# Kernel optimization log

Measured on AMD Instinct MI355X. Metric: run time of the kernel, lower is better.

The kernel has to match this reference:

```python
import jax, jax.numpy as jnp
import numpy as np
from jax import lax

B0, C0, H0, W0 = 4, 128, 48, 48
GR = 32  # growth rate
NL = 4   # dense layers


def conv1x1(x, w, b):
    # w: [O, Cin], x: [B, Cin, H, W]
    return jnp.einsum('oc,bchw->bohw', w, x) + b[None, :, None, None]


def conv3x3(x, w, b):
    y = lax.conv_general_dilated(x, w, (1, 1), [(1, 1), (1, 1)],
                                 dimension_numbers=('NCHW', 'OIHW', 'NCHW'))
    return y + b[None, :, None, None]


def batchnorm(x, g, b, eps=1e-5):
    # training-mode BatchNorm2d: batch statistics over (B, H, W)
    mu = jnp.mean(x, axis=(0, 2, 3), keepdims=True)
    var = jnp.var(x, axis=(0, 2, 3), keepdims=True)
    return (x - mu) * lax.rsqrt(var + eps) * g[None, :, None, None] + b[None, :, None, None]


def apply_rope(x):
    B, C, H, W = x.shape
    half = C // 2
    theta = 1.0 / (10000.0 ** (jnp.arange(half, dtype=x.dtype) / half))
    # pos_emb[h, w, j] = (h + w) * theta[j]
    pos = (jnp.arange(H, dtype=x.dtype)[:, None, None]
           + jnp.arange(W, dtype=x.dtype)[None, :, None]) * theta
    cos = jnp.cos(pos).transpose(2, 0, 1)  # [half, H, W]
    sin = jnp.sin(pos).transpose(2, 0, 1)
    xr = x.reshape(B, half, 2, H, W)
    x_re, x_im = xr[:, :, 0], xr[:, :, 1]
    rr = x_re * cos - x_im * sin
    ri = x_re * sin + x_im * cos
    return jnp.stack([rr, ri], axis=2).reshape(B, C, H, W)


def setup_inputs() -> dict:
    key = jax.random.key(0)
    ks = iter(jax.random.split(key, 64))
    def nrm(shape, s=0.05):
        return jax.random.normal(next(ks), shape, jnp.float32) * s
    C = C0
    dc = C + NL * GR  # 256 dense-block output channels
    hid = 4 * C
    d = {
        'x': jax.random.normal(next(ks), (B0, C0, H0, W0), jnp.float32),
        'r_w': nrm((C, C)), 'r_b': jnp.zeros((C,), jnp.float32),
        'k_w': nrm((C, C)), 'k_b': jnp.zeros((C,), jnp.float32),
        'v_w': nrm((C, C)), 'v_b': jnp.zeros((C,), jnp.float32),
        'wc1_w': nrm((C // 4, C, 3, 3)), 'wc1_b': jnp.zeros((C // 4,), jnp.float32),
        'wc2_w': nrm((C, C // 4)), 'wc2_b': jnp.zeros((C,), jnp.float32),
        'u': nrm((C,), 0.1),
        'sn1_w': nrm((dc // 4, dc)), 'sn1_b': jnp.zeros((dc // 4,), jnp.float32),
        'sn2_w': nrm((dc, dc // 4)), 'sn2_b': jnp.zeros((dc,), jnp.float32),
        'lb_w': nrm((C // 4, dc)), 'lb_b': jnp.zeros((C // 4,), jnp.float32),
        'ld_w': nrm((C // 4, dc)), 'ld_b': jnp.zeros((C // 4,), jnp.float32),
        'ps_w': nrm((C, C // 4)), 'ps_b': jnp.zeros((C,), jnp.float32),
        'pq_w': nrm((C, C)), 'pq_b': jnp.zeros((C,), jnp.float32),
        'fc1_w': nrm((hid, C)), 'fc1_b': jnp.zeros((hid,), jnp.float32),
        'fc2_w': nrm((C, hid)), 'fc2_b': jnp.zeros((C,), jnp.float32),
    }
    for i in range(NL):
        cin = C + i * GR
        d[f'db_g{i}'] = jnp.ones((cin,), jnp.float32)
        d[f'db_b{i}'] = jnp.zeros((cin,), jnp.float32)
        d[f'db_w{i}'] = nrm((GR, cin, 3, 3))
        d[f'db_cb{i}'] = jnp.zeros((GR,), jnp.float32)
    return d


def _forward(x, r_w, r_b, k_w, k_b, v_w, v_b, wc1_w, wc1_b, wc2_w, wc2_b, u,
             db_g0, db_b0, db_w0, db_cb0, db_g1, db_b1, db_w1, db_cb1,
             db_g2, db_b2, db_w2, db_cb2, db_g3, db_b3, db_w3, db_cb3,
             sn1_w, sn1_b, sn2_w, sn2_b, lb_w, lb_b, ld_w, ld_b,
             ps_w, ps_b, pq_w, pq_b, fc1_w, fc1_b, fc2_w, fc2_b):
    B, C, H, W = x.shape
    N = H * W
    # decay gate w (hidden is None so it multiplies zeros, kept for fidelity)
    w_gate = jax.nn.sigmoid(conv1x1(jax.nn.relu(conv3x3(x, wc1_w, wc1_b)), wc2_w, wc2_b)).reshape(B, C, N)
    x_rope = apply_rope(x)
    r = jax.nn.sigmoid(conv1x1(x, r_w, r_b))
    k = conv1x1(x_rope, k_w, k_b).reshape(B, C, N)
    v = conv1x1(x_rope, v_w, v_b).reshape(B, C, N)
    zeros = jnp.zeros_like(k)
    new_num = zeros * jnp.exp(-w_gate) + k * v
    new_den = zeros * jnp.exp(-w_gate) + k
    eu = jnp.exp(u)[None, :, None]
    wkv = ((new_num + eu * k * v) / (new_den + eu * k)).reshape(B, C, H, W)
    recursive_output = r * wkv
    # dense block (concat-growth)
    feats = x
    for g, bb, wt, cb in ((db_g0, db_b0, db_w0, db_cb0), (db_g1, db_b1, db_w1, db_cb1),
                          (db_g2, db_b2, db_w2, db_cb2), (db_g3, db_b3, db_w3, db_cb3)):
        h = jax.nn.relu(batchnorm(feats, g, bb))
        feats = jnp.concatenate([feats, conv3x3(h, wt, cb)], axis=1)
    df = feats  # [B, C+4*GR, H, W]
    # adaptive spiking neuron
    tau = jnp.mean(jax.nn.sigmoid(conv1x1(jax.nn.relu(conv1x1(df, sn1_w, sn1_b)), sn2_w, sn2_b)),
                   axis=(2, 3), keepdims=True)
    spike_prob = jax.nn.sigmoid((df - 1.0) * 5.0)
    sf = spike_prob * (df * jnp.exp(-1.0 / (tau + 1e-6))) + (1.0 - spike_prob) * df
    # first attention over N tokens, channels = C//4
    Bf = conv1x1(sf, lb_w, lb_b).reshape(B, -1, N)
    Df = conv1x1(sf, ld_w, ld_b).reshape(B, -1, N)
    attn = jax.nn.softmax(jnp.einsum('bcn,bcm->bnm', Bf, Bf), axis=-1)
    att1 = jnp.einsum('bnm,bcm->bcn', attn, Df).reshape(B, -1, H, W)
    spike_output = conv1x1(att1, ps_w, ps_b)
    combined = recursive_output + spike_output
    # second attention (k/v convs are shared with WKV path)
    Q = conv1x1(combined, pq_w, pq_b).reshape(B, C, N)
    K = conv1x1(combined, k_w, k_b).reshape(B, C, N)
    V = conv1x1(combined, v_w, v_b).reshape(B, C, N)
    scores = jnp.einsum('bcn,bcm->bnm', Q, K) / jnp.sqrt(jnp.asarray(C, x.dtype))
    aw = jax.nn.softmax(scores, axis=-1)
    att2 = jnp.einsum('bnm,bcm->bcn', aw, V).reshape(B, C, H, W)
    x1 = x + att2
    out = x1 + conv1x1(jax.nn.relu(conv1x1(x1, fc1_w, fc1_b)) ** 2, fc2_w, fc2_b)
    return out, new_num, new_den


def reference(x, r_w, r_b, k_w, k_b, v_w, v_b, wc1_w, wc1_b, wc2_w, wc2_b, u,
              db_g0, db_b0, db_w0, db_cb0, db_g1, db_b1, db_w1, db_cb1,
              db_g2, db_b2, db_w2, db_cb2, db_g3, db_b3, db_w3, db_cb3,
              sn1_w, sn1_b, sn2_w, sn2_b, lb_w, lb_b, ld_w, ld_b,
              ps_w, ps_b, pq_w, pq_b, fc1_w, fc1_b, fc2_w, fc2_b):
    return _forward(x, r_w, r_b, k_w, k_b, v_w, v_b, wc1_w, wc1_b, wc2_w, wc2_b, u,
                    db_g0, db_b0, db_w0, db_cb0, db_g1, db_b1, db_w1, db_cb1,
                    db_g2, db_b2, db_w2, db_cb2, db_g3, db_b3, db_w3, db_cb3,
                    sn1_w, sn1_b, sn2_w, sn2_b, lb_w, lb_b, ld_w, ld_b,
                    ps_w, ps_b, pq_w, pq_b, fc1_w, fc1_b, fc2_w, fc2_b)
```

## Files before the change

### kernel.cpp

```cpp
#include <hip/hip_runtime.h>
#include <math.h>

#define BB 4
#define CC 128
#define HH 48
#define WW 48
#define NSP (HH*WW)
#define DCC 256
#define BCN (BB*CC*NSP)
#define KS 4

typedef float f32x4 __attribute__((ext_vector_type(4)));
typedef __bf16 bf16x8 __attribute__((ext_vector_type(8)));
typedef __bf16 bf16x4 __attribute__((ext_vector_type(4)));

__device__ __forceinline__ float sigmf(float v) { return 1.0f / (1.0f + __expf(-v)); }

struct Prep {
  const float* wsrc[13];
  int wlen[13];
  int woff[13];
  const float* psrc[4];
  int pcin[4];
  int poff[4];
  const float* x;
  float* sums;
  float* sums2;
  __bf16* x_t;
  __bf16* xrope_t;
};
__global__ __launch_bounds__(256) void prep_kernel(Prep a, __bf16* __restrict__ wdst,
                                                   __bf16* __restrict__ pdst) {
  __shared__ float lds[32][33];
  __shared__ float rs[4], rs2[4];
  int g = blockIdx.y;
  int idx = blockIdx.x * 256 + threadIdx.x;
  if (g < 13) {
    if (idx < a.wlen[g]) wdst[a.woff[g] + idx] = (__bf16)a.wsrc[g][idx];
  } else if (g < 17) {
    int L = g - 13;
    int cin = a.pcin[L];
    if (idx < 9 * 32 * cin) {
      int c = idx % cin;
      int o = (idx / cin) % 32;
      int tap = idx / (cin * 32);
      pdst[a.poff[L] + idx] = (__bf16)a.psrc[L][((size_t)o * cin + c) * 9 + tap];
    }
  } else if (g == 17) {
    int c = blockIdx.x;
    if (c >= 128) return;
    float s = 0.f, s2 = 0.f;
    for (int i = threadIdx.x; i < BB * NSP; i += 256) {
      int b = i / NSP, n = i % NSP;
      float v = a.x[((size_t)b * 128 + c) * NSP + n];
      s += v;
      s2 += v * v;
    }
#pragma unroll
    for (int off = 32; off > 0; off >>= 1) {
      s += __shfl_down(s, off);
      s2 += __shfl_down(s2, off);
    }
    int wid = threadIdx.x >> 6;
    if ((threadIdx.x & 63) == 0) { rs[wid] = s; rs2[wid] = s2; }
    __syncthreads();
    if (threadIdx.x == 0) {
      a.sums[c] = rs[0] + rs[1] + rs[2] + rs[3];
      a.sums2[c] = rs2[0] + rs2[1] + rs2[2] + rs2[3];
    }
  } else {
    int T = (g - 18) * 256 + blockIdx.x;
    if (T >= 1152) return;
    int b = T / 288;
    int r = T % 288;
    int c0 = (r / 72) * 32;
    int n0 = (r % 72) * 32;
    int tid = threadIdx.x;
    int nn = tid & 31, cs = tid >> 5;
#pragma unroll
    for (int j = 0; j < 4; ++j) {
      int cc = c0 + cs * 4 + j;
      lds[cs * 4 + j][nn] = a.x[((size_t)b * 128 + cc) * NSP + n0 + nn];
    }
    __syncthreads();
    int c = tid & 31, ns = tid >> 5;
#pragma unroll
    for (int j = 0; j < 4; ++j) {
      int n2 = ns * 4 + j;
      float pv = lds[c][n2];
      a.x_t[((size_t)b * NSP + n0 + n2) * 128 + c0 + c] = (__bf16)pv;
      int gc = c0 + c;
      int i = gc >> 1;
      float re = lds[c & ~1][n2];
      float im = lds[c | 1][n2];
      int n = n0 + n2;
      int h = n / WW, w = n % WW;
      float theta = __expf(-9.2103403719761836f * ((float)i) / 64.0f);
      float pos = (float)(h + w) * theta;
      float cs_ = cosf(pos), sn_ = sinf(pos);
      float vr_ = (gc & 1) ? (re * sn_ + im * cs_) : (re * cs_ - im * sn_);
      a.xrope_t[((size_t)b * NSP + n0 + n2) * 128 + c0 + c] = (__bf16)vr_;
    }
  }
}

__global__ __launch_bounds__(256) void kvr_kernel(
    const __bf16* __restrict__ xrope_t, const __bf16* __restrict__ x_t,
    const __bf16* __restrict__ wk, const __bf16* __restrict__ wvp,
    const __bf16* __restrict__ wr,
    const float* __restrict__ k_b, const float* __restrict__ v_b,
    const float* __restrict__ r_b, const float* __restrict__ u,
    float* __restrict__ kden, float* __restrict__ knum, float* __restrict__ rec) {
  int tid = threadIdx.x;
  int wv = tid >> 6, lane = tid & 63;
  int m15 = lane & 15, quad = lane >> 4;
  int b = blockIdx.y;
  int n0 = blockIdx.x * 16;
  int o0 = wv * 32;
  int n = n0 + m15;
  const __bf16* brr = xrope_t + ((size_t)b * NSP + n) * 128 + quad * 8;
  const __bf16* brx = x_t + ((size_t)b * NSP + n) * 128 + quad * 8;
  const __bf16* ak0 = wk + (size_t)(o0 + m15) * 128 + quad * 8;
  const __bf16* ak1 = wk + (size_t)(o0 + 16 + m15) * 128 + quad * 8;
  const __bf16* av0 = wvp + (size_t)(o0 + m15) * 128 + quad * 8;
  const __bf16* av1 = wvp + (size_t)(o0 + 16 + m15) * 128 + quad * 8;
  const __bf16* ar0 = wr + (size_t)(o0 + m15) * 128 + quad * 8;
  const __bf16* ar1 = wr + (size_t)(o0 + 16 + m15) * 128 + quad * 8;
  f32x4 fk[2], fv[2], fr[2];
#pragma unroll
  for (int t = 0; t < 2; ++t) {
    fk[t] = (f32x4){0.f, 0.f, 0.f, 0.f};
    fv[t] = (f32x4){0.f, 0.f, 0.f, 0.f};
    fr[t] = (f32x4){0.f, 0.f, 0.f, 0.f};
  }
#pragma unroll
  for (int kc = 0; kc < 128; kc += 32) {
    bf16x8 br_ = *(const bf16x8*)(brr + kc);
    bf16x8 bx_ = *(const bf16x8*)(brx + kc);
    fk[0] = __builtin_amdgcn_mfma_f32_16x16x32_bf16(*(const bf16x8*)(ak0 + kc), br_, fk[0], 0, 0, 0);
    fk[1] = __builtin_amdgcn_mfma_f32_16x16x32_bf16(*(const bf16x8*)(ak1 + kc), br_, fk[1], 0, 0, 0);
    fv[0] = __builtin_amdgcn_mfma_f32_16x16x32_bf16(*(const bf16x8*)(av0 + kc), br_, fv[0], 0, 0, 0);
    fv[1] = __builtin_amdgcn_mfma_f32_16x16x32_bf16(*(const bf16x8*)(av1 + kc), br_, fv[1], 0, 0, 0);
    fr[0] = __builtin_amdgcn_mfma_f32_16x16x32_bf16(*(const bf16x8*)(ar0 + kc), bx_, fr[0], 0, 0, 0);
    fr[1] = __builtin_amdgcn_mfma_f32_16x16x32_bf16(*(const bf16x8*)(ar1 + kc), bx_, fr[1], 0, 0, 0);
  }
#pragma unroll
  for (int t = 0; t < 2; ++t) {
#pragma unroll
    for (int reg = 0; reg < 4; ++reg) {
      int ol = o0 + t * 16 + quad * 4 + reg;
      float kk = fk[t][reg] + k_b[ol];
      float vv = fv[t][reg] + v_b[ol];
      float rr = sigmf(fr[t][reg] + r_b[ol]);
      float eu = __expf(u[ol]);
      size_t idx = ((size_t)b * 128 + ol) * NSP + n;
      float nv = kk * vv, tt = eu * kk;
      kden[idx] = kk;
      knum[idx] = nv;
      rec[idx] = rr * ((nv + tt * vv) / (kk + tt));
    }
  }
}

template <int OUT>
__device__ __forceinline__ void gemm_store(void* outp, int b, int n, int Oseg,
                                           int obase, int quad, const float* vr) {
  if (OUT == 0) {
    float* op = (float*)outp;
#pragma unroll
    for (int reg = 0; reg < 4; ++reg)
      op[((size_t)b * Oseg + obase + quad * 4 + reg) * NSP + n] = vr[reg];
  } else if (OUT == 1) {
    __bf16* op = (__bf16*)outp;
    bf16x4 pk;
#pragma unroll
    for (int reg = 0; reg < 4; ++reg) pk[reg] = (__bf16)vr[reg];
    *(bf16x4*)(op + ((size_t)b * NSP + n) * Oseg + obase + quad * 4) = pk;
  } else {
    __bf16* op = (__bf16*)outp;
#pragma unroll
    for (int reg = 0; reg < 4; ++reg)
      op[((size_t)b * Oseg + obase + quad * 4 + reg) * NSP + n] = (__bf16)vr[reg];
  }
}

template <int K, int ACT, int OUT0, int OUT1, int OUT2, int SPLITB>
__global__ __launch_bounds__(256) void gemm_mfma_kernel(
    const __bf16* __restrict__ in_t, const __bf16* __restrict__ in_t2,
    const __bf16* __restrict__ wb,
    const float* __restrict__ bias0, const float* __restrict__ bias1,
    const float* __restrict__ bias2,
    const float* __restrict__ add0, const float* __restrict__ add1,
    void* __restrict__ out0, void* __restrict__ out1, void* __restrict__ out2,
    int osplit, int osplit2, int Ototal, float sc0, float sc1, float sc2) {
  int tid = threadIdx.x;
  int wv = tid >> 6, lane = tid & 63;
  int m15 = lane & 15, quad = lane >> 4;
  int b = blockIdx.y;
  int n0 = blockIdx.x * 16;
  int wpb = blockDim.x >> 6;
  int o0 = (blockIdx.z * wpb + wv) * 32;
  if (o0 >= Ototal) return;
  int n = n0 + m15;
  const __bf16* brow = in_t + ((size_t)b * NSP + n) * (SPLITB ? 128 : K) + quad * 8;
  const __bf16* brow2 = SPLITB ? (in_t2 + ((size_t)b * NSP + n) * 128 + quad * 8) : nullptr;
  const __bf16* a0p = wb + (size_t)(o0 + m15) * K + quad * 8;
  const __bf16* a1p = wb + (size_t)(o0 + 16 + m15) * K + quad * 8;
  f32x4 of0 = (f32x4){0.f, 0.f, 0.f, 0.f};
  f32x4 of1 = (f32x4){0.f, 0.f, 0.f, 0.f};
#pragma unroll
  for (int kc = 0; kc < K; kc += 32) {
    bf16x8 bfr;
    if constexpr (SPLITB) {
      bfr = (kc < 128) ? *(const bf16x8*)(brow + kc) : *(const bf16x8*)(brow2 + (kc - 128));
    } else {
      bfr = *(const bf16x8*)(brow + kc);
    }
    bf16x8 a0 = *(const bf16x8*)(a0p + kc);
    bf16x8 a1 = *(const bf16x8*)(a1p + kc);
    of0 = __builtin_amdgcn_mfma_f32_16x16x32_bf16(a0, bfr, of0, 0, 0, 0);
    of1 = __builtin_amdgcn_mfma_f32_16x16x32_bf16(a1, bfr, of1, 0, 0, 0);
  }
  int seg = (o0 >= osplit2) ? 2 : (o0 >= osplit) ? 1 : 0;
  int segb = (seg == 2) ? osplit2 : (seg == 1) ? osplit : 0;
  int sege = (seg == 2) ? Ototal : (seg == 1) ? osplit2 : osplit;
  int Oseg = sege - segb;
  int ol0 = o0 - segb;
  const float* bias = (seg == 2) ? bias2 : (seg == 1) ? bias1 : bias0;
  const float* add = (seg == 2) ? nullptr : (seg == 1) ? add1 : add0;
  void* outp = (seg == 2) ? out2 : (seg == 1) ? out1 : out0;
  float sc = (seg == 2) ? sc2 : (seg == 1) ? sc1 : sc0;
#pragma unroll
  for (int t = 0; t < 2; ++t) {
    f32x4 acc = t ? of1 : of0;
    float vr[4];
#pragma unroll
    for (int reg = 0; reg < 4; ++reg) {
      int ol = ol0 + t * 16 + quad * 4 + reg;
      float v = acc[reg] + bias[ol];
      if (ACT == 1) v = fmaxf(v, 0.0f);
      else if (ACT == 2) v = sigmf(v);
      else if (ACT == 3) { v = fmaxf(v, 0.0f); v = v * v; }
      v *= sc;
      if (add) v += add[((size_t)b * Oseg + ol) * NSP + n];
      vr[reg] = v;
    }
    if constexpr (OUT0 == 3) {
#pragma unroll
      for (int reg = 0; reg < 4; ++reg) {
        float sv = vr[reg];
        sv += __shfl_xor(sv, 1);
        sv += __shfl_xor(sv, 2);
        sv += __shfl_xor(sv, 4);
        sv += __shfl_xor(sv, 8);
        if (m15 == 0)
          ((float*)out0)[((size_t)(b * DCC + ol0 + t * 16 + quad * 4 + reg)) * 144 +
                         blockIdx.x] = sv;
      }
    } else {
      if (seg == 0) gemm_store<OUT0>(outp, b, n, Oseg, ol0 + t * 16, quad, vr);
      else if (seg == 1) gemm_store<OUT1>(outp, b, n, Oseg, ol0 + t * 16, quad, vr);
      else gemm_store<OUT2>(outp, b, n, Oseg, ol0 + t * 16, quad, vr);
    }
  }
}

__global__ __launch_bounds__(128) void lbld_sf_kernel(
    const __bf16* __restrict__ x_t, const __bf16* __restrict__ dense_t,
    const float* __restrict__ taupart, const __bf16* __restrict__ wlb,
    const float* __restrict__ lb_b, const float* __restrict__ ld_b,
    __bf16* __restrict__ Bft, __bf16* __restrict__ Dfb) {
  __shared__ float ef[256];
  int tid = threadIdx.x;
  int b = blockIdx.y;
  for (int ch = tid; ch < 256; ch += 128) {
    const f32x4* tp = (const f32x4*)(taupart + ((size_t)(b * DCC + ch)) * 144);
    f32x4 s4 = (f32x4){0.f, 0.f, 0.f, 0.f};
#pragma unroll
    for (int j = 0; j < 36; ++j) s4 += tp[j];
    float tv = (s4.x + s4.y + s4.z + s4.w) * (1.0f / (float)NSP);
    ef[ch] = __expf(-1.0f / (tv + 1e-6f)) - 1.0f;
  }
  __syncthreads();
  int wv = tid >> 6, lane = tid & 63;
  int m15 = lane & 15, quad = lane >> 4;
  int n0 = blockIdx.x * 16;
  int o0 = wv * 32;
  int n = n0 + m15;
  const __bf16* bx = x_t + ((size_t)b * NSP + n) * 128 + quad * 8;
  const __bf16* bd = dense_t + ((size_t)b * NSP + n) * 128 + quad * 8;
  const __bf16* a0p = wlb + (size_t)(o0 + m15) * 256 + quad * 8;
  const __bf16* a1p = wlb + (size_t)(o0 + 16 + m15) * 256 + quad * 8;
  f32x4 of0 = (f32x4){0.f, 0.f, 0.f, 0.f};
  f32x4 of1 = (f32x4){0.f, 0.f, 0.f, 0.f};
#pragma unroll
  for (int kc = 0; kc < 256; kc += 32) {
    bf16x8 raw = (kc < 128) ? *(const bf16x8*)(bx + kc) : *(const bf16x8*)(bd + (kc - 128));
    bf16x8 sfv;
#pragma unroll
    for (int j = 0; j < 8; ++j) {
      float df = (float)raw[j];
      float sp = sigmf((df - 1.0f) * 5.0f);
      sfv[j] = (__bf16)(df * (1.0f + sp * ef[kc + quad * 8 + j]));
    }
    bf16x8 a0 = *(const bf16x8*)(a0p + kc);
    bf16x8 a1 = *(const bf16x8*)(a1p + kc);
    of0 = __builtin_amdgcn_mfma_f32_16x16x32_bf16(a0, sfv, of0, 0, 0, 0);
    of1 = __builtin_amdgcn_mfma_f32_16x16x32_bf16(a1, sfv, of1, 0, 0, 0);
  }
  if (o0 == 0) {
#pragma unroll
    for (int t = 0; t < 2; ++t) {
      f32x4 acc = t ? of1 : of0;
      bf16x4 pk;
#pragma unroll
      for (int reg = 0; reg < 4; ++reg) pk[reg] = (__bf16)(acc[reg] + lb_b[t * 16 + quad * 4 + reg]);
      *(bf16x4*)(Bft + ((size_t)b * NSP + n) * 32 + t * 16 + quad * 4) = pk;
    }
  } else {
#pragma unroll
    for (int t = 0; t < 2; ++t) {
      f32x4 acc = t ? of1 : of0;
#pragma unroll
      for (int reg = 0; reg < 4; ++reg) {
        int ol = t * 16 + quad * 4 + reg;
        Dfb[((size_t)b * 32 + ol) * NSP + n] = (__bf16)(acc[reg] + ld_b[ol]);
      }
    }
  }
}

template <int Cin>
__global__ __launch_bounds__(256) void convbn_kernel(
    const __bf16* __restrict__ x_t, const __bf16* __restrict__ dense_t,
    const __bf16* __restrict__ wb, const float* __restrict__ cb,
    float* __restrict__ sums, float* __restrict__ sums2,
    const float* __restrict__ cpart_in,
    const float* __restrict__ g, const float* __restrict__ bbp,
    __bf16* __restrict__ dense_out, float* __restrict__ cpart_out, int cout0) {
  constexpr int KCin = Cin / 32;
  constexpr int NIT = 9 * KCin;
  __shared__ float red[4][64][8];
  __shared__ float scsh[2][Cin];
  __shared__ float tred[64][4];
  __shared__ float fin[64];
  int tid = threadIdx.x;
  const float inv = 1.0f / (float)(BB * NSP);

  if (cpart_in) {
    int row = tid >> 2, sl = tid & 3;
    const f32x4* cp = (const f32x4*)(cpart_in + (size_t)row * 576 + sl * 144);
    f32x4 s4 = (f32x4){0.f, 0.f, 0.f, 0.f};
#pragma unroll
    for (int j = 0; j < 36; ++j) s4 += cp[j];
    tred[row][sl] = s4.x + s4.y + s4.z + s4.w;
    __syncthreads();
    if (tid < 64) fin[tid] = tred[tid][0] + tred[tid][1] + tred[tid][2] + tred[tid][3];
    __syncthreads();
    if (blockIdx.x == 0 && blockIdx.y == 0 && tid < 32) {
      sums[Cin - 32 + tid] = fin[tid];
      sums2[Cin - 32 + tid] = fin[32 + tid];
    }
  }
  for (int ch = tid; ch < Cin; ch += 256) {
    float S, S2;
    if (cpart_in && ch >= Cin - 32) {
      S = fin[ch - (Cin - 32)];
      S2 = fin[ch - (Cin - 32) + 32];
    } else {
      S = sums[ch];
      S2 = sums2[ch];
    }
    float m = S * inv;
    float var = S2 * inv - m * m;
    float sc_ = rsqrtf(var + 1e-5f) * g[ch];
    scsh[0][ch] = sc_;
    scsh[1][ch] = bbp[ch] - m * sc_;
  }
  __syncthreads();

  int wv = tid >> 6, lane = tid & 63;
  int m15 = lane & 15, quad = lane >> 4;
  int b = blockIdx.y;
  int n0 = blockIdx.x * 16;
  int n = n0 + m15;
  int h = n / WW, w = n % WW;
  f32x4 of0 = (f32x4){0.f, 0.f, 0.f, 0.f};
  f32x4 of1 = (f32x4){0.f, 0.f, 0.f, 0.f};
  const __bf16* bx_ = x_t + (size_t)b * NSP * 128;
  const __bf16* bd_ = dense_t + (size_t)b * NSP * 128;
  const bf16x8 zf = {};
  int begin = (wv * NIT) / 4, end = ((wv + 1) * NIT) / 4;
  int cur = -1;
  float bsc[8], bsh[8];
  const __bf16* base = nullptr;
  for (int ci = begin; ci < end; ++ci) {
    int chunk = ci / 9;
    int tap = ci - chunk * 9;
    int kc = chunk * 32;
    if (chunk != cur) {
      cur = chunk;
      int cc = kc + quad * 8;
#pragma unroll
      for (int j = 0; j < 8; ++j) {
        bsc[j] = scsh[0][cc + j];
        bsh[j] = scsh[1][cc + j];
      }
      base = (cc < 128) ? (bx_ + cc) : (bd_ + cc - 128);
    }
    int dh = tap / 3 - 1, dw = tap % 3 - 1;
    bool valid = ((unsigned)(h + dh) < HH) && ((unsigned)(w + dw) < WW);
    int pa = valid ? (n + dh * WW + dw) : 0;
    bf16x8 raw = *(const bf16x8*)(base + (size_t)pa * 128);
    bf16x8 bfr;
#pragma unroll
    for (int j = 0; j < 8; ++j) {
      float v = fmaxf((float)raw[j] * bsc[j] + bsh[j], 0.0f);
      bfr[j] = (__bf16)v;
    }
    if (!valid) bfr = zf;
    const __bf16* wt = wb + (size_t)tap * 32 * Cin + kc + quad * 8;
    bf16x8 a0 = *(const bf16x8*)(wt + (size_t)m15 * Cin);
    bf16x8 a1 = *(const bf16x8*)(wt + (size_t)(16 + m15) * Cin);
    of0 = __builtin_amdgcn_mfma_f32_16x16x32_bf16(a0, bfr, of0, 0, 0, 0);
    of1 = __builtin_amdgcn_mfma_f32_16x16x32_bf16(a1, bfr, of1, 0, 0, 0);
  }
  float* myred = red[wv][lane];
#pragma unroll
  for (int reg = 0; reg < 4; ++reg) {
    myred[reg] = of0[reg];
    myred[4 + reg] = of1[reg];
  }
  __syncthreads();
  if (wv == 0) {
    int dloc = cout0 - 128;
    __bf16* dt = dense_out + ((size_t)b * NSP + n) * 128 + dloc;
    bf16x4 pk0, pk1;
    float sv[4][4];
#pragma unroll
    for (int reg = 0; reg < 4; ++reg) {
      int o = quad * 4 + reg;
      float v0 = red[0][lane][reg] + red[1][lane][reg] + red[2][lane][reg] +
                 red[3][lane][reg] + cb[o];
      float v1 = red[0][lane][4 + reg] + red[1][lane][4 + reg] + red[2][lane][4 + reg] +
                 red[3][lane][4 + reg] + cb[16 + o];
      pk0[reg] = (__bf16)v0;
      pk1[reg] = (__bf16)v1;
      sv[reg][0] = v0;
      sv[reg][1] = v0 * v0;
      sv[reg][2] = v1;
      sv[reg][3] = v1 * v1;
    }
    *(bf16x4*)(dt + quad * 4) = pk0;
    *(bf16x4*)(dt + 16 + quad * 4) = pk1;
    if (cpart_out) {
#pragma unroll
      for (int reg = 0; reg < 4; ++reg) {
        float a0 = sv[reg][0], q0 = sv[reg][1], a1 = sv[reg][2], q1 = sv[reg][3];
#pragma unroll
        for (int mk = 1; mk < 16; mk <<= 1) {
          a0 += __shfl_xor(a0, mk);
          q0 += __shfl_xor(q0, mk);
          a1 += __shfl_xor(a1, mk);
          q1 += __shfl_xor(q1, mk);
        }
        if (m15 == 0) {
          int o = quad * 4 + reg;
          int pidx = blockIdx.y * 144 + blockIdx.x;
          cpart_out[(size_t)o * 576 + pidx] = a0;
          cpart_out[(size_t)(32 + o) * 576 + pidx] = q0;
          cpart_out[(size_t)(16 + o) * 576 + pidx] = a1;
          cpart_out[(size_t)(48 + o) * 576 + pidx] = q1;
        }
      }
    }
  }
}

template <int CD>
__global__ __launch_bounds__(256) void attn_part_kernel(
    const __bf16* __restrict__ Qt, const __bf16* __restrict__ Kt,
    const __bf16* __restrict__ Vb, __bf16* __restrict__ Op,
    float* __restrict__ lp) {
  constexpr int NC = CD / 16;
  constexpr int KC = CD / 32;
  constexpr int KEYS = NSP / KS;
  constexpr int KP = CD + 4;
  constexpr int VP = 36;
  __shared__ __bf16 kl[32][KP];
  __shared__ __bf16 vl[CD][VP];
  int tid = threadIdx.x;
  int wv = tid >> 6, lane = tid & 63;
  int m15 = lane & 15, quad = lane >> 4;
  int b = blockIdx.y, ks = blockIdx.z;
  int n0 = blockIdx.x * 64 + wv * 16;

  bf16x8 qf[KC];
  const __bf16* qrow = Qt + ((size_t)b * NSP + n0 + m15) * CD + quad * 8;
#pragma unroll
  for (int kc = 0; kc < KC; ++kc) qf[kc] = *(const bf16x8*)(qrow + kc * 32);

  f32x4 of[NC];
#pragma unroll
  for (int i = 0; i < NC; ++i) of[i] = (f32x4){0.f, 0.f, 0.f, 0.f};
  float lsum = 0.f;

  const __bf16* Kb = Kt + (size_t)b * NSP * CD;
  const __bf16* Vbb = Vb + (size_t)b * CD * NSP;

  for (int m0 = ks * KEYS; m0 < (ks + 1) * KEYS; m0 += 32) {
    __syncthreads();
    for (int i = tid; i < 32 * CD / 8; i += 256) {
      int row = i / (CD / 8);
      int cc8 = (i % (CD / 8)) * 8;
      *(bf16x8*)&kl[row][cc8] = *(const bf16x8*)(Kb + (size_t)(m0 + row) * CD + cc8);
    }
    for (int i = tid; i < CD * 4; i += 256) {
      int ch = i / 4;
      int k8 = (i % 4) * 8;
      *(bf16x8*)&vl[ch][k8] = *(const bf16x8*)(Vbb + (size_t)ch * NSP + m0 + k8);
    }
    __syncthreads();
    f32x4 s[2];
#pragma unroll
    for (int t = 0; t < 2; ++t) {
      f32x4 acc = (f32x4){0.f, 0.f, 0.f, 0.f};
#pragma unroll
      for (int kc = 0; kc < KC; ++kc) {
        bf16x8 kf = *(const bf16x8*)&kl[t * 16 + m15][kc * 32 + quad * 8];
        acc = __builtin_amdgcn_mfma_f32_16x16x32_bf16(kf, qf[kc], acc, 0, 0, 0);
      }
      s[t] = acc;
    }
    bf16x8 pf;
#pragma unroll
    for (int t = 0; t < 2; ++t) {
#pragma unroll
      for (int r = 0; r < 4; ++r) {
        float ev = __expf(s[t][r]);
        lsum += ev;
        pf[t * 4 + r] = (__bf16)ev;
      }
    }
#pragma unroll
    for (int ct = 0; ct < NC; ++ct) {
      bf16x4 va = *(const bf16x4*)&vl[ct * 16 + m15][4 * quad];
      bf16x4 vb_ = *(const bf16x4*)&vl[ct * 16 + m15][16 + 4 * quad];
      bf16x8 vf;
#pragma unroll
      for (int j = 0; j < 4; ++j) { vf[j] = va[j]; vf[4 + j] = vb_[j]; }
      of[ct] = __builtin_amdgcn_mfma_f32_16x16x32_bf16(pf, vf, of[ct], 0, 0, 0);
    }
  }

  lsum += __shfl_xor(lsum, 16);
  lsum += __shfl_xor(lsum, 32);
  float* lpb = lp + (size_t)(ks * BB + b) * NSP + n0;
  if (quad == 0) lpb[m15] = lsum;
  __bf16* Ob = Op + (size_t)(ks * BB + b) * CD * NSP;
#pragma unroll
  for (int ct = 0; ct < NC; ++ct) {
    bf16x4 pk;
#pragma unroll
    for (int reg = 0; reg < 4; ++reg) pk[reg] = (__bf16)of[ct][reg];
    *(bf16x4*)(Ob + (size_t)(ct * 16 + m15) * NSP + n0 + quad * 4) = pk;
  }
}

__global__ __launch_bounds__(256) void combine32_kernel(const __bf16* __restrict__ Op,
                                                        const float* __restrict__ lp,
                                                        __bf16* __restrict__ att1_t) {
  __shared__ float lds[32][33];
  int b = blockIdx.z;
  int n0 = blockIdx.x * 32;
  int tid = threadIdx.x;
  int nn = tid & 31, cs = tid >> 5;
  float ltot = 0.f;
#pragma unroll
  for (int ks = 0; ks < KS; ++ks) ltot += lp[(size_t)(ks * BB + b) * NSP + n0 + nn];
  float linv = 1.0f / ltot;
#pragma unroll
  for (int j = 0; j < 4; ++j) {
    int cc = cs * 4 + j;
    float s = 0.f;
#pragma unroll
    for (int ks = 0; ks < KS; ++ks)
      s += (float)Op[((size_t)(ks * BB + b) * 32 + cc) * NSP + n0 + nn];
    lds[cc][nn] = s * linv;
  }
  __syncthreads();
  int c = tid & 31, ns = tid >> 5;
#pragma unroll
  for (int j = 0; j < 4; ++j) {
    int n2 = ns * 4 + j;
    att1_t[((size_t)b * NSP + n0 + n2) * 32 + c] = (__bf16)lds[c][n2];
  }
}

__global__ __launch_bounds__(256) void combine128_kernel(
    const __bf16* __restrict__ Op, const float* __restrict__ lp,
    const float* __restrict__ x, float* __restrict__ x1, __bf16* __restrict__ x1_t) {
  __shared__ float lds[32][33];
  int b = blockIdx.z;
  int n0 = blockIdx.x * 32;
  int c0 = blockIdx.y * 32;
  int tid = threadIdx.x;
  int nn = tid & 31, cs = tid >> 5;
  float ltot = 0.f;
#pragma unroll
  for (int ks = 0; ks < KS; ++ks) ltot += lp[(size_t)(ks * BB + b) * NSP + n0 + nn];
  float linv = 1.0f / ltot;
#pragma unroll
  for (int j = 0; j < 4; ++j) {
    int gc = c0 + cs * 4 + j;
    float s = 0.f;
#pragma unroll
    for (int ks = 0; ks < KS; ++ks)
      s += (float)Op[((size_t)(ks * BB + b) * CC + gc) * NSP + n0 + nn];
    float v = s * linv + x[((size_t)b * CC + gc) * NSP + n0 + nn];
    lds[cs * 4 + j][nn] = v;
    x1[((size_t)b * CC + gc) * NSP + n0 + nn] = v;
  }
  __syncthreads();
  int c = tid & 31, ns = tid >> 5;
#pragma unroll
  for (int j = 0; j < 4; ++j) {
    int n2 = ns * 4 + j;
    x1_t[((size_t)b * NSP + n0 + n2) * CC + c0 + c] = (__bf16)lds[c][n2];
  }
}

extern "C" void kernel_launch(void* const* d_in, const int* in_sizes, int n_in,
                              void* d_out, int out_size, void* d_ws, size_t ws_size,
                              hipStream_t stream) {
  const float* x = (const float*)d_in[0];
  const float* r_w = (const float*)d_in[1];
  const float* r_b = (const float*)d_in[2];
  const float* k_w = (const float*)d_in[3];
  const float* k_b = (const float*)d_in[4];
  const float* v_w = (const float*)d_in[5];
  const float* v_b = (const float*)d_in[6];
  const float* u = (const float*)d_in[11];
  const float* sn1_w = (const float*)d_in[12];
  const float* sn1_b = (const float*)d_in[13];
  const float* sn2_w = (const float*)d_in[14];
  const float* sn2_b = (const float*)d_in[15];
  const float* lb_w = (const float*)d_in[16];
  const float* lb_b = (const float*)d_in[17];
  const float* ld_w = (const float*)d_in[18];
  const float* ld_b = (const float*)d_in[19];
  const float* ps_w = (const float*)d_in[20];
  const float* ps_b = (const float*)d_in[21];
  const float* pq_w = (const float*)d_in[22];
  const float* pq_b = (const float*)d_in[23];
  const float* fc1_w = (const float*)d_in[24];
  const float* fc1_b = (const float*)d_in[25];
  const float* fc2_w = (const float*)d_in[26];
  const float* fc2_b = (const float*)d_in[27];
  const float* db_g[4] = {(const float*)d_in[28], (const float*)d_in[32],
                          (const float*)d_in[36], (const float*)d_in[40]};
  const float* db_b[4] = {(const float*)d_in[29], (const float*)d_in[33],
                          (const float*)d_in[37], (const float*)d_in[41]};
  const float* db_w[4] = {(const float*)d_in[30], (const float*)d_in[34],
                          (const float*)d_in[38], (const float*)d_in[42]};
  const float* db_cb[4] = {(const float*)d_in[31], (const float*)d_in[35],
                           (const float*)d_in[39], (const float*)d_in[43]};

  float* outp = (float*)d_out;
  float* knum = outp + BCN;
  float* kden = outp + 2 * (size_t)BCN;

  float* ws = (float*)d_ws;
  const size_t F_FEATS = 0;
  const size_t F_REC = 4718592;
  const size_t F_V = 5898240;
  const size_t F_R = 7077888;
  const size_t F_XR = 8257536;
  const size_t F_XT = 8847360;
  const size_t F_DFB = 9437184;
  const size_t F_AT1T = 9584640;
  const size_t F_CT = 9732096;
  const size_t F_LP = 10321920;
  const size_t F_WB = 10434048;
  const size_t F_WB3 = 10575360;
  const size_t F_STATS = 10676736;
  const size_t F_TAUP = 10714112;
  float* sums = ws + F_STATS;
  float* sums2 = ws + F_STATS + 256;
  float* cpart0 = ws + F_FEATS;
  float* cpart1 = cpart0 + 36864;
  float* cpart2 = cpart1 + 36864;
  float* taupart = ws + F_TAUP;
  float* lp = ws + F_LP;
  __bf16* wbase = (__bf16*)(ws + F_WB);
  __bf16* wb3 = (__bf16*)(ws + F_WB3);
  const int W_KV = 0;
  const int W_R = 32768;
  const int W_SN1 = 49152;
  const int W_SN2 = 65536;
  const int W_LBLD = 81920;
  const int W_PS = 98304;
  const int W_PQK = 102400;
  const int W_FC1 = 151552;
  const int W_FC2 = 217088;
  const int W3_OFF[4] = {0, 36864, 82944, 138240};

  dim3 blk(256);
  __bf16* xrope_t = (__bf16*)(ws + F_XR);
  __bf16* x_t = (__bf16*)(ws + F_XT);

  Prep pp;
  pp.wsrc[0] = k_w;    pp.wlen[0] = 16384; pp.woff[0] = W_KV;
  pp.wsrc[1] = v_w;    pp.wlen[1] = 16384; pp.woff[1] = W_KV + 16384;
  pp.wsrc[2] = r_w;    pp.wlen[2] = 16384; pp.woff[2] = W_R;
  pp.wsrc[3] = sn1_w;  pp.wlen[3] = 16384; pp.woff[3] = W_SN1;
  pp.wsrc[4] = sn2_w;  pp.wlen[4] = 16384; pp.woff[4] = W_SN2;
  pp.wsrc[5] = lb_w;   pp.wlen[5] = 8192;  pp.woff[5] = W_LBLD;
  pp.wsrc[6] = ld_w;   pp.wlen[6] = 8192;  pp.woff[6] = W_LBLD + 8192;
  pp.wsrc[7] = ps_w;   pp.wlen[7] = 4096;  pp.woff[7] = W_PS;
  pp.wsrc[8] = pq_w;   pp.wlen[8] = 16384; pp.woff[8] = W_PQK;
  pp.wsrc[9] = k_w;    pp.wlen[9] = 16384; pp.woff[9] = W_PQK + 16384;
  pp.wsrc[10] = v_w;   pp.wlen[10] = 16384; pp.woff[10] = W_PQK + 32768;
  pp.wsrc[11] = fc1_w; pp.wlen[11] = 65536; pp.woff[11] = W_FC1;
  pp.wsrc[12] = fc2_w; pp.wlen[12] = 65536; pp.woff[12] = W_FC2;
  for (int i = 0; i < 4; ++i) {
    pp.psrc[i] = db_w[i];
    pp.pcin[i] = 128 + 32 * i;
    pp.poff[i] = W3_OFF[i];
  }
  pp.x = x;
  pp.sums = sums;
  pp.sums2 = sums2;
  pp.x_t = x_t;
  pp.xrope_t = xrope_t;
  prep_kernel<<<dim3(256, 23), blk, 0, stream>>>(pp, wbase, wb3);

  kvr_kernel<<<dim3(144, 4), blk, 0, stream>>>(
      xrope_t, x_t, wbase + W_KV, wbase + W_KV + 16384, wbase + W_R,
      k_b, v_b, r_b, u, kden, knum, ws + F_REC);

  __bf16* dense_t = (__bf16*)(ws + F_R);
  convbn_kernel<128><<<dim3(144, 4), blk, 0, stream>>>(
      x_t, dense_t, wb3 + W3_OFF[0], db_cb[0], sums, sums2, nullptr,
      db_g[0], db_b[0], dense_t, cpart0, 128);
  convbn_kernel<160><<<dim3(144, 4), blk, 0, stream>>>(
      x_t, dense_t, wb3 + W3_OFF[1], db_cb[1], sums, sums2, cpart0,
      db_g[1], db_b[1], dense_t, cpart1, 160);
  convbn_kernel<192><<<dim3(144, 4), blk, 0, stream>>>(
      x_t, dense_t, wb3 + W3_OFF[2], db_cb[2], sums, sums2, cpart1,
      db_g[2], db_b[2], dense_t, cpart2, 192);
  convbn_kernel<224><<<dim3(144, 4), blk, 0, stream>>>(
      x_t, dense_t, wb3 + W3_OFF[3], db_cb[3], sums, sums2, cpart2,
      db_g[3], db_b[3], dense_t, nullptr, 224);

  __bf16* z1_t = (__bf16*)(ws + F_XR);
  gemm_mfma_kernel<256, 1, 1, 1, 0, 1><<<dim3(144, 4, 1), dim3(128), 0, stream>>>(
      x_t, dense_t, wbase + W_SN1, sn1_b, sn1_b, nullptr, nullptr, nullptr,
      z1_t, z1_t, nullptr, 64, 64, 64, 1.f, 1.f, 1.f);
  gemm_mfma_kernel<64, 2, 3, 3, 0, 0><<<dim3(144, 4, 2), blk, 0, stream>>>(
      z1_t, nullptr, wbase + W_SN2, sn2_b, sn2_b, nullptr, nullptr, nullptr,
      taupart, taupart, nullptr, 256, 256, 256, 1.f, 1.f, 1.f);
  __bf16* Bft = (__bf16*)(ws + F_CT + 294912);
  __bf16* Dfb = (__bf16*)(ws + F_DFB);
  lbld_sf_kernel<<<dim3(144, 4), dim3(128), 0, stream>>>(
      x_t, dense_t, taupart, wbase + W_LBLD, lb_b, ld_b, Bft, Dfb);
  __bf16* Opart = (__bf16*)(ws + F_FEATS);
  attn_part_kernel<32><<<dim3(36, 4, KS), blk, 0, stream>>>(Bft, Bft, Dfb, Opart, lp);
  __bf16* att1_t = (__bf16*)(ws + F_AT1T);
  combine32_kernel<<<dim3(72, 1, 4), blk, 0, stream>>>(Opart, lp, att1_t);
  __bf16* comb_t = (__bf16*)(ws + F_CT);
  gemm_mfma_kernel<32, 0, 1, 1, 0, 0><<<dim3(144, 4, 1), blk, 0, stream>>>(
      att1_t, nullptr, wbase + W_PS, ps_b, ps_b, nullptr, ws + F_REC, ws + F_REC,
      comb_t, comb_t, nullptr, 128, 128, 128, 1.f, 1.f, 1.f);

  __bf16* Qt = (__bf16*)(ws + F_XR);
  __bf16* K2t = (__bf16*)(ws + F_XT);
  __bf16* V2b = (__bf16*)(ws + F_V);
  gemm_mfma_kernel<128, 0, 1, 1, 2, 0><<<dim3(144, 4, 3), blk, 0, stream>>>(
      comb_t, nullptr, wbase + W_PQK, pq_b, k_b, v_b, nullptr, nullptr,
      Qt, K2t, V2b, 128, 256, 384, 0.08838834764831845f, 1.f, 1.f);
  attn_part_kernel<128><<<dim3(36, 4, KS), blk, 0, stream>>>(Qt, K2t, V2b, Opart, lp);
  float* x1 = ws + F_R;
  __bf16* x1_t = (__bf16*)(ws + F_CT);
  combine128_kernel<<<dim3(72, 4, 4), blk, 0, stream>>>(Opart, lp, x, x1, x1_t);

  __bf16* h_t = (__bf16*)(ws + F_FEATS);
  gemm_mfma_kernel<128, 3, 1, 1, 0, 0><<<dim3(144, 4, 4), blk, 0, stream>>>(
      x1_t, nullptr, wbase + W_FC1, fc1_b, fc1_b, nullptr, nullptr, nullptr,
      h_t, h_t, nullptr, 512, 512, 512, 1.f, 1.f, 1.f);
  gemm_mfma_kernel<512, 0, 0, 0, 0, 0><<<dim3(144, 4, 1), blk, 0, stream>>>(
      h_t, nullptr, wbase + W_FC2, fc2_b, fc2_b, nullptr, x1, x1,
      outp, outp, nullptr, 128, 128, 128, 1.f, 1.f, 1.f);
}
```

Measured before the change: 405.9 us.

## Fuse SN1+SN2 squeeze GEMMs and combine32 with PS projection GEMM

```diff
diff --git a/kernel.cpp b/kernel.cpp
--- a/kernel.cpp
+++ b/kernel.cpp
@@ -245,22 +245,78 @@
       if (add) v += add[((size_t)b * Oseg + ol) * NSP + n];
       vr[reg] = v;
     }
-    if constexpr (OUT0 == 3) {
+    if (seg == 0) gemm_store<OUT0>(outp, b, n, Oseg, ol0 + t * 16, quad, vr);
+    else if (seg == 1) gemm_store<OUT1>(outp, b, n, Oseg, ol0 + t * 16, quad, vr);
+    else gemm_store<OUT2>(outp, b, n, Oseg, ol0 + t * 16, quad, vr);
+  }
+}
+
+__global__ __launch_bounds__(256) void sn12_kernel(
+    const __bf16* __restrict__ x_t, const __bf16* __restrict__ dense_t,
+    const __bf16* __restrict__ wsn1, const float* __restrict__ sn1_b,
+    const __bf16* __restrict__ wsn2, const float* __restrict__ sn2_b,
+    float* __restrict__ taupart) {
+  __shared__ __bf16 z1l[16][72];
+  int tid = threadIdx.x;
+  int wv = tid >> 6, lane = tid & 63;
+  int m15 = lane & 15, quad = lane >> 4;
+  int b = blockIdx.y;
+  int n0 = blockIdx.x * 16;
+  int n = n0 + m15;
+  if (wv < 2) {
+    int o0 = wv * 32;
+    const __bf16* bx = x_t + ((size_t)b * NSP + n) * 128 + quad * 8;
+    const __bf16* bd = dense_t + ((size_t)b * NSP + n) * 128 + quad * 8;
+    const __bf16* a0p = wsn1 + (size_t)(o0 + m15) * 256 + quad * 8;
+    const __bf16* a1p = wsn1 + (size_t)(o0 + 16 + m15) * 256 + quad * 8;
+    f32x4 of0 = (f32x4){0.f, 0.f, 0.f, 0.f};
+    f32x4 of1 = (f32x4){0.f, 0.f, 0.f, 0.f};
+#pragma unroll
+    for (int kc = 0; kc < 256; kc += 32) {
+      bf16x8 bfr = (kc < 128) ? *(const bf16x8*)(bx + kc) : *(const bf16x8*)(bd + (kc - 128));
+      bf16x8 a0 = *(const bf16x8*)(a0p + kc);
+      bf16x8 a1 = *(const bf16x8*)(a1p + kc);
+      of0 = __builtin_amdgcn_mfma_f32_16x16x32_bf16(a0, bfr, of0, 0, 0, 0);
+      of1 = __builtin_amdgcn_mfma_f32_16x16x32_bf16(a1, bfr, of1, 0, 0, 0);
+    }
+#pragma unroll
+    for (int t = 0; t < 2; ++t) {
+      f32x4 acc = t ? of1 : of0;
 #pragma unroll
       for (int reg = 0; reg < 4; ++reg) {
-        float sv = vr[reg];
+        int ol = o0 + t * 16 + quad * 4 + reg;
+        z1l[m15][ol] = (__bf16)fmaxf(acc[reg] + sn1_b[ol], 0.0f);
+      }
+    }
+  }
+  __syncthreads();
+  bf16x8 bfr0 = *(const bf16x8*)&z1l[m15][quad * 8];
+  bf16x8 bfr1 = *(const bf16x8*)&z1l[m15][32 + quad * 8];
+#pragma unroll
+  for (int ot = 0; ot < 2; ++ot) {
+    int o0 = (wv * 2 + ot) * 32;
+    const __bf16* a0p = wsn2 + (size_t)(o0 + m15) * 64 + quad * 8;
+    const __bf16* a1p = wsn2 + (size_t)(o0 + 16 + m15) * 64 + quad * 8;
+    f32x4 of0 = (f32x4){0.f, 0.f, 0.f, 0.f};
+    f32x4 of1 = (f32x4){0.f, 0.f, 0.f, 0.f};
+    of0 = __builtin_amdgcn_mfma_f32_16x16x32_bf16(*(const bf16x8*)(a0p), bfr0, of0, 0, 0, 0);
+    of0 = __builtin_amdgcn_mfma_f32_16x16x32_bf16(*(const bf16x8*)(a0p + 32), bfr1, of0, 0, 0, 0);
+    of1 = __builtin_amdgcn_mfma_f32_16x16x32_bf16(*(const bf16x8*)(a1p), bfr0, of1, 0, 0, 0);
+    of1 = __builtin_amdgcn_mfma_f32_16x16x32_bf16(*(const bf16x8*)(a1p + 32), bfr1, of1, 0, 0, 0);
+#pragma unroll
+    for (int t = 0; t < 2; ++t) {
+      f32x4 acc = t ? of1 : of0;
+#pragma unroll
+      for (int reg = 0; reg < 4; ++reg) {
+        int ol = o0 + t * 16 + quad * 4 + reg;
+        float sv = sigmf(acc[reg] + sn2_b[ol]);
         sv += __shfl_xor(sv, 1);
         sv += __shfl_xor(sv, 2);
         sv += __shfl_xor(sv, 4);
         sv += __shfl_xor(sv, 8);
         if (m15 == 0)
-          ((float*)out0)[((size_t)(b * DCC + ol0 + t * 16 + quad * 4 + reg)) * 144 +
-                         blockIdx.x] = sv;
+          taupart[((size_t)(b * DCC + ol)) * 144 + blockIdx.x] = sv;
       }
-    } else {
-      if (seg == 0) gemm_store<OUT0>(outp, b, n, Oseg, ol0 + t * 16, quad, vr);
-      else if (seg == 1) gemm_store<OUT1>(outp, b, n, Oseg, ol0 + t * 16, quad, vr);
-      else gemm_store<OUT2>(outp, b, n, Oseg, ol0 + t * 16, quad, vr);
     }
   }
 }
@@ -567,11 +623,12 @@
   }
 }
 
-__global__ __launch_bounds__(256) void combine32_kernel(const __bf16* __restrict__ Op,
-                                                        const float* __restrict__ lp,
-                                                        __bf16* __restrict__ att1_t) {
+__global__ __launch_bounds__(256) void c32ps_kernel(
+    const __bf16* __restrict__ Op, const float* __restrict__ lp,
+    const __bf16* __restrict__ wps, const float* __restrict__ ps_b,
+    const float* __restrict__ rec, __bf16* __restrict__ comb_t) {
   __shared__ float lds[32][33];
-  int b = blockIdx.z;
+  int b = blockIdx.y;
   int n0 = blockIdx.x * 32;
   int tid = threadIdx.x;
   int nn = tid & 31, cs = tid >> 5;
@@ -589,11 +646,34 @@
     lds[cc][nn] = s * linv;
   }
   __syncthreads();
-  int c = tid & 31, ns = tid >> 5;
-#pragma unroll
-  for (int j = 0; j < 4; ++j) {
-    int n2 = ns * 4 + j;
-    att1_t[((size_t)b * NSP + n0 + n2) * 32 + c] = (__bf16)lds[c][n2];
+  int wv = tid >> 6, lane = tid & 63;
+  int m15 = lane & 15, quad = lane >> 4;
+  int o0 = wv * 32;
+  bf16x8 a0 = *(const bf16x8*)(wps + (size_t)(o0 + m15) * 32 + quad * 8);
+  bf16x8 a1 = *(const bf16x8*)(wps + (size_t)(o0 + 16 + m15) * 32 + quad * 8);
+#pragma unroll
+  for (int t2 = 0; t2 < 2; ++t2) {
+    int nl = t2 * 16 + m15;
+    int n = n0 + nl;
+    bf16x8 bfr;
+#pragma unroll
+    for (int j = 0; j < 8; ++j) bfr[j] = (__bf16)lds[quad * 8 + j][nl];
+    f32x4 of0 = (f32x4){0.f, 0.f, 0.f, 0.f};
+    f32x4 of1 = (f32x4){0.f, 0.f, 0.f, 0.f};
+    of0 = __builtin_amdgcn_mfma_f32_16x16x32_bf16(a0, bfr, of0, 0, 0, 0);
+    of1 = __builtin_amdgcn_mfma_f32_16x16x32_bf16(a1, bfr, of1, 0, 0, 0);
+#pragma unroll
+    for (int t = 0; t < 2; ++t) {
+      f32x4 acc = t ? of1 : of0;
+      bf16x4 pk;
+#pragma unroll
+      for (int reg = 0; reg < 4; ++reg) {
+        int ol = o0 + t * 16 + quad * 4 + reg;
+        float v = acc[reg] + ps_b[ol] + rec[((size_t)b * 128 + ol) * NSP + n];
+        pk[reg] = (__bf16)v;
+      }
+      *(bf16x4*)(comb_t + ((size_t)b * NSP + n) * 128 + o0 + t * 16 + quad * 4) = pk;
+    }
   }
 }
 
@@ -753,25 +833,17 @@
       x_t, dense_t, wb3 + W3_OFF[3], db_cb[3], sums, sums2, cpart2,
       db_g[3], db_b[3], dense_t, nullptr, 224);
 
-  __bf16* z1_t = (__bf16*)(ws + F_XR);
-  gemm_mfma_kernel<256, 1, 1, 1, 0, 1><<<dim3(144, 4, 1), dim3(128), 0, stream>>>(
-      x_t, dense_t, wbase + W_SN1, sn1_b, sn1_b, nullptr, nullptr, nullptr,
-      z1_t, z1_t, nullptr, 64, 64, 64, 1.f, 1.f, 1.f);
-  gemm_mfma_kernel<64, 2, 3, 3, 0, 0><<<dim3(144, 4, 2), blk, 0, stream>>>(
-      z1_t, nullptr, wbase + W_SN2, sn2_b, sn2_b, nullptr, nullptr, nullptr,
-      taupart, taupart, nullptr, 256, 256, 256, 1.f, 1.f, 1.f);
+  sn12_kernel<<<dim3(144, 4), blk, 0, stream>>>(
+      x_t, dense_t, wbase + W_SN1, sn1_b, wbase + W_SN2, sn2_b, taupart);
   __bf16* Bft = (__bf16*)(ws + F_CT + 294912);
   __bf16* Dfb = (__bf16*)(ws + F_DFB);
   lbld_sf_kernel<<<dim3(144, 4), dim3(128), 0, stream>>>(
       x_t, dense_t, taupart, wbase + W_LBLD, lb_b, ld_b, Bft, Dfb);
   __bf16* Opart = (__bf16*)(ws + F_FEATS);
   attn_part_kernel<32><<<dim3(36, 4, KS), blk, 0, stream>>>(Bft, Bft, Dfb, Opart, lp);
-  __bf16* att1_t = (__bf16*)(ws + F_AT1T);
-  combine32_kernel<<<dim3(72, 1, 4), blk, 0, stream>>>(Opart, lp, att1_t);
   __bf16* comb_t = (__bf16*)(ws + F_CT);
-  gemm_mfma_kernel<32, 0, 1, 1, 0, 0><<<dim3(144, 4, 1), blk, 0, stream>>>(
-      att1_t, nullptr, wbase + W_PS, ps_b, ps_b, nullptr, ws + F_REC, ws + F_REC,
-      comb_t, comb_t, nullptr, 128, 128, 128, 1.f, 1.f, 1.f);
+  c32ps_kernel<<<dim3(72, 4), blk, 0, stream>>>(
+      Opart, lp, wbase + W_PS, ps_b, ws + F_REC, comb_t);
 
   __bf16* Qt = (__bf16*)(ws + F_XR);
   __bf16* K2t = (__bf16*)(ws + F_XT);
```

New measurement: 405.5 us. No clear change (-0.1%).
